# Optimization experiments

Measured on AMD Instinct MI355X. Metric: run time of the kernel, lower is better.

The kernel has to match this reference:

```python
import jax, jax.numpy as jnp
from jax import lax
import numpy as np

B, T, S, Q = 256, 128, 16, 16
E, K = 128, 20
VOCAB = 50000 + K  # vocab_size + num_blocks (key slots appended)


def prelu(x, a):
    return jnp.where(x > 0, x, a * x)


def setup_inputs() -> dict:
    key = jax.random.key(0)
    ks = jax.random.split(key, 12)
    story = jax.random.randint(ks[0], (B, T, S), 0, 50000, dtype=jnp.int64 if jax.config.jax_enable_x64 else jnp.int32)
    query = jax.random.randint(ks[1], (B, Q), 0, 50000, dtype=jnp.int64 if jax.config.jax_enable_x64 else jnp.int32)
    embed_table = jax.random.normal(ks[2], (VOCAB, E), jnp.float32) * 0.1
    embed_table = embed_table.at[0].set(0.0)  # padding_idx=0
    story_mask = jnp.ones((S, E), jnp.float32)
    query_mask = jnp.ones((Q, E), jnp.float32)
    prelu_a = jnp.ones((E,), jnp.float32)
    U = jax.random.normal(ks[3], (E, E), jnp.float32) * 0.1
    V = jax.random.normal(ks[4], (E, E), jnp.float32) * 0.1
    W = jax.random.normal(ks[5], (E, E), jnp.float32) * 0.1
    bias = jax.random.normal(ks[6], (E,), jnp.float32) * 0.1
    H = jax.random.normal(ks[7], (E, E), jnp.float32) * 0.1
    R = jax.random.normal(ks[8], (VOCAB, E), jnp.float32) * 0.1
    return {"story": story, "query": query, "embed_table": embed_table,
            "story_mask": story_mask, "query_mask": query_mask, "prelu_a": prelu_a,
            "U": U, "V": V, "W": W, "bias": bias, "H": H, "R": R}


def reference(story, query, embed_table, story_mask, query_mask, prelu_a, U, V, W, bias, H, R):
    # encode story: (B,T,S,E) * (S,E) summed over S -> (B,T,E)
    s_enc = jnp.sum(embed_table[story] * story_mask, axis=2)
    # encode query: (B,Q,E) * (Q,E) summed over Q -> (B,E)
    q_enc = jnp.sum(embed_table[query] * query_mask, axis=1)

    keys = embed_table[VOCAB - K:]              # (K,E) block keys
    state0 = jnp.broadcast_to(keys[None], (B, K, E))
    key_V = keys @ V.T                           # (K,E), loop-invariant

    def step(state, x):                          # state (B,K,E), x (B,E)
        gate = jax.nn.sigmoid(jnp.einsum('be,bke->bk', x, state) + x @ keys.T)  # (B,K)
        cand = prelu(jnp.einsum('bke,fe->bkf', state, U) + bias
                     + (x @ W.T)[:, None, :] + key_V[None], prelu_a)
        ns = state + gate[..., None] * cand
        norm = jnp.linalg.norm(ns, axis=-1, keepdims=True) + 1e-8
        ns = jnp.where(ns > 0, ns, 1.0) / norm   # Threshold(0,1) then L2-normalize
        return ns, None

    state, _ = lax.scan(step, state0, jnp.swapaxes(s_enc, 0, 1))  # scan over T

    # output module
    att = jax.nn.softmax(jnp.einsum('bke,be->bk', state, q_enc), axis=-1)
    u = jnp.einsum('bk,bke->be', att, state)
    y = prelu(q_enc + u @ H.T, prelu_a) @ R.T    # (B,VOCAB)
    return y
```

## Files before the change

kernel.cpp:

```cpp
#include <hip/hip_runtime.h>
#include <hip/hip_bf16.h>
#include <stdint.h>

#define BB 256
#define TT 128
#define SS 16
#define QQ 16
#define EE 128
#define KK 20
#define VOCAB 50020
#define KB_ROWS 10
#define XK_STR 24

#define NCVT  3127
#define NSTORY (BB*TT/8)
#define NQUERY (BB/8)

typedef __attribute__((ext_vector_type(8))) _Float16 h8v;
typedef __attribute__((ext_vector_type(2))) __fp16 fp2v;
typedef __attribute__((ext_vector_type(4))) unsigned short u4h;
typedef __attribute__((ext_vector_type(4))) float f4v;
#define MFMA16(a,b,c) __builtin_amdgcn_mfma_f32_16x16x32_f16(a,b,c,0,0,0)

static __device__ __forceinline__ unsigned pk2u(fp2v h){
  union { fp2v h; unsigned u; } c; c.h = h; return c.u;
}
static __device__ __forceinline__ float pk_lo(fp2v h){ return (float)h[0]; }
static __device__ __forceinline__ float pk_hi(fp2v h){ return (float)h[1]; }
static __device__ __forceinline__ unsigned short h1u(_Float16 h){
  union { _Float16 h; unsigned short u; } c; c.h = h; return c.u;
}
static __device__ __forceinline__ void split2_8(const float* v, h8v& h, h8v& l){
  #pragma unroll
  for (int j=0;j<8;++j){
    _Float16 hb = (_Float16)v[j];
    float hf = (float)hb;
    h[j] = hb;
    l[j] = (_Float16)(v[j]-hf);
  }
}
static __device__ __forceinline__ float dpp_add16(float x){
  int v;
  v = __builtin_amdgcn_update_dpp(0, __float_as_int(x), 0xB1, 0xF, 0xF, true);
  x += __int_as_float(v);
  v = __builtin_amdgcn_update_dpp(0, __float_as_int(x), 0x4E, 0xF, 0xF, true);
  x += __int_as_float(v);
  v = __builtin_amdgcn_update_dpp(0, __float_as_int(x), 0x124, 0xF, 0xF, true);
  x += __int_as_float(v);
  v = __builtin_amdgcn_update_dpp(0, __float_as_int(x), 0x128, 0xF, 0xF, true);
  x += __int_as_float(v);
  return x;
}
template<int IMM>
static __device__ __forceinline__ u4h tr_read(unsigned va){
  u4h d;
  asm volatile("ds_read_b64_tr_b16 %0, %1 offset:%c2" : "=v"(d) : "v"(va), "i"(IMM));
  return d;
}
static __device__ __forceinline__ h8v cat8h(u4h a, u4h b){
  union { u4h p[2]; h8v v; } u; u.p[0]=a; u.p[1]=b; return u.v;
}
#define LDA(P,K4) cat8h(tr_read<(P)*4096+(K4)*1024>(va), tr_read<(P)*4096+(K4)*1024+128>(va))

static const size_t OFF_SENC = 0;
static const size_t OFF_QENC = OFF_SENC + (size_t)BB*TT*EE;
static const size_t OFF_CKF  = OFF_QENC + (size_t)BB*EE;
static const size_t OFF_XW   = OFF_CKF  + (size_t)KK*EE;
static const size_t OFF_Z    = OFF_XW   + (size_t)BB*TT*EE;
static const size_t OFF_XK   = OFF_Z    + (size_t)BB*EE;
static const size_t OFF_ST   = OFF_XK   + (size_t)BB*TT*XK_STR;
static const size_t OFF_RH   = OFF_ST   + (size_t)BB*KK*EE;

__global__ __launch_bounds__(256) void k_pro(
    const int* __restrict__ story, const int* __restrict__ query,
    const float* __restrict__ emb, const float* __restrict__ smask,
    const float* __restrict__ qmask, const float* __restrict__ V,
    const float* __restrict__ bias, const float* __restrict__ R,
    float* __restrict__ senc, float* __restrict__ qenc,
    float* __restrict__ Ckf, unsigned short* __restrict__ Rh)
{
  int bid = blockIdx.x;
  int tid = threadIdx.x;
  if (bid < NCVT){
    size_t i = ((size_t)bid*256 + tid)*8;
    if (i >= (size_t)VOCAB*EE) return;
    float tmp[8];
    *(float4*)&tmp[0] = *(const float4*)(R+i);
    *(float4*)&tmp[4] = *(const float4*)(R+i+4);
    h8v h;
    #pragma unroll
    for (int j=0;j<8;++j) h[j] = (_Float16)tmp[j];
    *(h8v*)(Rh+i) = h;
  } else if (bid < NCVT + NSTORY){
    int row = (bid - NCVT)*8 + (tid>>5);
    int e4 = (tid&31)*4;
    float4 acc = make_float4(0.f,0.f,0.f,0.f);
    #pragma unroll
    for (int s=0; s<SS; ++s) {
      int id = story[(size_t)row*SS + s];
      float4 ev = *(const float4*)(emb + (size_t)id*EE + e4);
      float4 mv = *(const float4*)(smask + s*EE + e4);
      acc.x += ev.x*mv.x; acc.y += ev.y*mv.y; acc.z += ev.z*mv.z; acc.w += ev.w*mv.w;
    }
    *(float4*)(senc + (size_t)row*EE + e4) = acc;
  } else if (bid < NCVT + NSTORY + NQUERY){
    int row = (bid - NCVT - NSTORY)*8 + (tid>>5);
    int e4 = (tid&31)*4;
    float4 acc = make_float4(0.f,0.f,0.f,0.f);
    #pragma unroll
    for (int s=0; s<QQ; ++s) {
      int id = query[(size_t)row*QQ + s];
      float4 ev = *(const float4*)(emb + (size_t)id*EE + e4);
      float4 mv = *(const float4*)(qmask + s*EE + e4);
      acc.x += ev.x*mv.x; acc.y += ev.y*mv.y; acc.z += ev.z*mv.z; acc.w += ev.w*mv.w;
    }
    *(float4*)(qenc + (size_t)row*EE + e4) = acc;
  } else {
    int k = bid - NCVT - NSTORY - NQUERY;
    if (tid < 128){
      int f = tid;
      const float* key = emb + (size_t)(VOCAB-KK+k)*EE;
      const float* vr  = V + (size_t)f*EE;
      float acc = bias[f];
      for (int e=0; e<EE; e+=4) {
        float4 kv = *(const float4*)(key + e);
        float4 vv = *(const float4*)(vr + e);
        acc += kv.x*vv.x + kv.y*vv.y + kv.z*vv.z + kv.w*vv.w;
      }
      Ckf[k*EE + f] = acc;
    }
  }
}

__global__ __launch_bounds__(256) void k_xw(
    const float* __restrict__ senc, const float* __restrict__ W,
    const float* __restrict__ emb, float* __restrict__ xw,
    float* __restrict__ xk)
{
  __shared__ float xs[64*EE];
  __shared__ float keys_s[KK*EE];
  int tid = threadIdx.x;
  int r0 = blockIdx.x*64;
  for (int i=0;i<8;++i){
    int idx = tid + i*256; int r = idx>>5; int c4 = (idx&31)*4;
    *(float4*)(xs + r*EE + c4) = *(const float4*)(senc + (size_t)(r0+r)*EE + c4);
  }
  for (int idx=tid; idx<KK*EE; idx+=256)
    keys_s[idx] = emb[(size_t)(VOCAB-KK + (idx>>7))*EE + (idx&127)];
  __syncthreads();
  int f  = tid & 127;
  int rh = tid >> 7;
  float acc[32];
  #pragma unroll
  for (int i=0;i<32;++i) acc[i]=0.f;
  const float* wr = W + (size_t)f*EE;
  for (int e4=0; e4<EE; e4+=4) {
    float4 w4 = *(const float4*)(wr + e4);
    #pragma unroll
    for (int rr=0; rr<32; ++rr) {
      float4 x4 = *(const float4*)(xs + (rh*32+rr)*EE + e4);
      acc[rr] += w4.x*x4.x + w4.y*x4.y + w4.z*x4.z + w4.w*x4.w;
    }
  }
  #pragma unroll
  for (int rr=0; rr<32; ++rr)
    xw[(size_t)(r0 + rh*32 + rr)*EE + f] = acc[rr];
  for (int i=0;i<5;++i){
    int task = tid + i*256;
    int r = task/KK, k = task - r*KK;
    float a = 0.f;
    for (int e=0; e<EE; e+=4){
      float4 x4 = *(const float4*)(xs + r*EE + e);
      float4 k4 = *(const float4*)(keys_s + k*EE + e);
      a += x4.x*k4.x + x4.y*k4.y + x4.z*k4.z + x4.w*k4.w;
    }
    int ki = k < 10 ? k : k + 2;
    xk[(size_t)(r0+r)*XK_STR + ki] = a;
  }
}

struct ScanLds {
  unsigned short st[2][2][EE][16];
  unsigned short xp[2][2][EE];
  float npart[2][4][16];
};

__global__ __launch_bounds__(256) void k_scan(
    const float* __restrict__ emb, const float* __restrict__ U,
    const float* __restrict__ senc, const float* __restrict__ xw,
    const float* __restrict__ xk, const float* __restrict__ Ckf,
    const float* __restrict__ prelu_a, float* __restrict__ zst)
{
  __shared__ ScanLds L;
  int tid = threadIdx.x;
  int bid = blockIdx.x;
  int b   = bid >> 1, kb = bid & 1;
  int l   = tid & 63, cg = tid >> 6;
  int q   = l >> 4,  c  = l & 15;
  int col[2] = { cg*32 + c, cg*32 + 16 + c };

  for (int idx = tid; idx < 2*2*EE*16; idx += 256) ((unsigned short*)L.st)[idx] = 0;
  __syncthreads();
  for (int idx = tid; idx < KB_ROWS*EE; idx += 256){
    int row = idx >> 7, e = idx & 127;
    float v = emb[(size_t)(VOCAB - KK + kb*KB_ROWS + row)*EE + e];
    _Float16 hb = (_Float16)v;
    _Float16 lb = (_Float16)(v - (float)hb);
    L.st[0][0][e][row] = h1u(hb);
    L.st[0][1][e][row] = h1u(lb);
  }
  h8v bh[2][4], bl[2][4];
  #pragma unroll
  for (int nt=0;nt<2;++nt)
    #pragma unroll
    for (int kk=0;kk<4;++kk){
      float tmp[8];
      const float* up = U + (size_t)col[nt]*EE + kk*32 + q*8;
      *(float4*)&tmp[0] = *(const float4*)up;
      *(float4*)&tmp[4] = *(const float4*)(up+4);
      split2_8(tmp, bh[nt][kk], bl[nt][kk]);
    }
  float Creg[2][4], pa2[2], nsv[2][4];
  bool realr[4];
  #pragma unroll
  for (int r=0;r<4;++r) realr[r] = (4*q + r) < KB_ROWS;
  #pragma unroll
  for (int nt=0;nt<2;++nt){
    pa2[nt] = prelu_a[col[nt]];
    #pragma unroll
    for (int r=0;r<4;++r){
      int lr = 4*q + r;
      Creg[nt][r] = realr[r] ? Ckf[(kb*KB_ROWS+lr)*EE + col[nt]] : 0.f;
      nsv[nt][r]  = realr[r] ? emb[(size_t)(VOCAB-KK+kb*KB_ROWS+lr)*EE + col[nt]] : 0.f;
    }
  }

  const float* xrow  = senc + (size_t)b*TT*EE;
  const float* xwrow = xw   + (size_t)b*TT*EE;
  const float* xkrow = xk   + (size_t)b*TT*XK_STR + kb*12;

  if (tid < EE){
    float v = xrow[tid];
    _Float16 hb = (_Float16)v;
    _Float16 lb = (_Float16)(v - (float)hb);
    L.xp[0][0][tid] = h1u(hb); L.xp[0][1][tid] = h1u(lb);
  }
  float xwc[2] = { xwrow[col[0]], xwrow[col[1]] };
  float xkc[4];
  {
    f4v xk4 = {0.f,0.f,0.f,0.f};
    if (q < 3) xk4 = *(const f4v*)(xkrow + 4*q);
    #pragma unroll
    for (int r=0;r<4;++r) xkc[r] = realr[r] ? xk4[r] : 0.f;
  }

  unsigned va0 = (unsigned)(uintptr_t)&L.st[0][0][0][0] + q*256 + c*8;
  __syncthreads();

  for (int t=0; t<TT; ++t){
    int p = t & 1, pn = p ^ 1;
    unsigned va = va0 + p*8192;
    const unsigned short (*xpp)[EE] = L.xp[p];

    float invr[4];
    if (t > 0){
      f4v p0 = *(const f4v*)&L.npart[p][0][4*q];
      f4v p1 = *(const f4v*)&L.npart[p][1][4*q];
      f4v p2 = *(const f4v*)&L.npart[p][2][4*q];
      f4v p3 = *(const f4v*)&L.npart[p][3][4*q];
      f4v ss = p0 + p1 + p2 + p3;
      #pragma unroll
      for (int r=0;r<4;++r)
        invr[r] = __builtin_amdgcn_rcpf(__builtin_amdgcn_sqrtf(ss[r]) + 1e-8f);
    } else {
      #pragma unroll
      for (int r=0;r<4;++r) invr[r] = 1.0f;
    }

    float nxv = 0.f, xwn[2] = {0.f,0.f};
    f4v xk4n = {0.f,0.f,0.f,0.f};
    if (t+1 < TT){
      if (tid < EE) nxv = xrow[(size_t)(t+1)*EE + tid];
      xwn[0] = xwrow[(size_t)(t+1)*EE + col[0]];
      xwn[1] = xwrow[(size_t)(t+1)*EE + col[1]];
      if (q < 3) xk4n = *(const f4v*)(xkrow + (size_t)(t+1)*XK_STR + 4*q);
    }

    h8v Ah[4] = { LDA(0,0), LDA(0,1), LDA(0,2), LDA(0,3) };
    h8v Al[4] = { LDA(1,0), LDA(1,1), LDA(1,2), LDA(1,3) };
    asm volatile("s_waitcnt lgkmcnt(0)" ::: "memory");
    __builtin_amdgcn_sched_barrier(0);

    f4v z4 = {0.f,0.f,0.f,0.f};
    f4v acc[2][2] = {{z4,z4},{z4,z4}};
    f4v gac[2] = {z4,z4};
    #pragma unroll
    for (int kk=0; kk<4; ++kk){
      int h = kk>>1;
      h8v xh = *(const h8v*)&xpp[0][kk*32 + q*8];
      h8v xl = *(const h8v*)&xpp[1][kk*32 + q*8];
      #pragma unroll
      for (int nt=0;nt<2;++nt){
        acc[nt][h] = MFMA16(Al[kk], bh[nt][kk], acc[nt][h]);
        acc[nt][h] = MFMA16(Ah[kk], bl[nt][kk], acc[nt][h]);
        acc[nt][h] = MFMA16(Ah[kk], bh[nt][kk], acc[nt][h]);
      }
      gac[h] = MFMA16(Al[kk], xh, gac[h]);
      gac[h] = MFMA16(Ah[kk], xl, gac[h]);
      gac[h] = MFMA16(Ah[kk], xh, gac[h]);
    }
    f4v acc0 = acc[0][0] + acc[0][1];
    f4v acc1 = acc[1][0] + acc[1][1];
    f4v gacc = gac[0] + gac[1];

    float s2[4];
    #pragma unroll
    for (int r=0;r<4;++r){
      float graw = gacc[r]*invr[r] + xkc[r];
      float g = __builtin_amdgcn_rcpf(1.0f + __builtin_amdgcn_exp2f(-1.442695040889f * graw));
      float s2r = 0.f;
      #pragma unroll
      for (int nt=0;nt<2;++nt){
        float so = nsv[nt][r] * invr[r];
        float cv = (nt ? acc1[r] : acc0[r])*invr[r] + Creg[nt][r] + xwc[nt];
        cv = cv > 0.f ? cv : pa2[nt]*cv;
        float n = so + g*cv;
        nsv[nt][r] = realr[r] ? (n > 0.f ? n : 1.0f) : 0.f;
        s2r += n*n;
      }
      s2[r] = dpp_add16(s2r);
    }
    if (c == 0){
      f4v np; np[0]=s2[0]; np[1]=s2[1]; np[2]=s2[2]; np[3]=s2[3];
      *(f4v*)&L.npart[pn][cg][4*q] = np;
    }

    #pragma unroll
    for (int nt=0;nt<2;++nt){
      float v0=nsv[nt][0], v1=nsv[nt][1], v2=nsv[nt][2], v3=nsv[nt][3];
      fp2v pa = __builtin_amdgcn_cvt_pkrtz(v0, v1);
      fp2v pb = __builtin_amdgcn_cvt_pkrtz(v2, v3);
      float r0 = v0 - pk_lo(pa);
      float r1 = v1 - pk_hi(pa);
      float r2 = v2 - pk_lo(pb);
      float r3 = v3 - pk_hi(pb);
      fp2v pc = __builtin_amdgcn_cvt_pkrtz(r0, r1);
      fp2v pd = __builtin_amdgcn_cvt_pkrtz(r2, r3);
      *(uint2*)&L.st[pn][0][col[nt]][4*q] = make_uint2(pk2u(pa), pk2u(pb));
      *(uint2*)&L.st[pn][1][col[nt]][4*q] = make_uint2(pk2u(pc), pk2u(pd));
    }
    if (t+1 < TT && tid < EE){
      _Float16 hb = (_Float16)nxv;
      _Float16 lb = (_Float16)(nxv - (float)hb);
      L.xp[pn][0][tid] = h1u(hb); L.xp[pn][1][tid] = h1u(lb);
    }
    xwc[0]=xwn[0]; xwc[1]=xwn[1];
    #pragma unroll
    for (int r=0;r<4;++r) xkc[r] = realr[r] ? xk4n[r] : 0.f;
    __syncthreads();
  }

  {
    int pf = TT & 1;
    f4v p0 = *(const f4v*)&L.npart[pf][0][4*q];
    f4v p1 = *(const f4v*)&L.npart[pf][1][4*q];
    f4v p2 = *(const f4v*)&L.npart[pf][2][4*q];
    f4v p3 = *(const f4v*)&L.npart[pf][3][4*q];
    f4v ss = p0 + p1 + p2 + p3;
    #pragma unroll
    for (int r=0;r<4;++r){
      if (realr[r]){
        float inv = __builtin_amdgcn_rcpf(__builtin_amdgcn_sqrtf(ss[r]) + 1e-8f);
        #pragma unroll
        for (int nt=0;nt<2;++nt)
          zst[((size_t)b*KK + kb*KB_ROWS + 4*q + r)*EE + col[nt]] = nsv[nt][r]*inv;
      }
    }
  }
}

__global__ __launch_bounds__(128) void k_tail(
    const float* __restrict__ zst, const float* __restrict__ qenc,
    const float* __restrict__ prelu_a, const float* __restrict__ H,
    float* __restrict__ zout)
{
  __shared__ float st[KK*EE];
  __shared__ float us[EE];
  __shared__ float red[2][KK];
  __shared__ float gs[KK];
  int b = blockIdx.x, tid = threadIdx.x;
  for (int i = tid; i < KK*EE; i += 128) st[i] = zst[(size_t)b*KK*EE + i];
  float qv = qenc[(size_t)b*EE + tid];
  __syncthreads();
  int wv = tid >> 6, ln = tid & 63;
  for (int k=0;k<KK;++k){
    float p = qv * st[k*EE + tid];
    #pragma unroll
    for (int off=32; off; off>>=1) p += __shfl_xor(p, off);
    if (ln == 0) red[wv][k] = p;
  }
  __syncthreads();
  if (tid == 0){
    float mx = -1e30f, gg[KK];
    for (int k=0;k<KK;++k){ float v = red[0][k]+red[1][k]; gg[k]=v; mx = fmaxf(mx, v); }
    float s = 0.f;
    for (int k=0;k<KK;++k){ float e_ = expf(gg[k]-mx); gg[k]=e_; s += e_; }
    for (int k=0;k<KK;++k) gs[k] = gg[k]/s;
  }
  __syncthreads();
  float u_ = 0.f;
  #pragma unroll
  for (int k=0;k<KK;++k) u_ += gs[k]*st[k*EE + tid];
  us[tid] = u_;
  __syncthreads();
  float hp = 0.f;
  const float* hr = H + (size_t)tid*EE;
  for (int e=0; e<EE; e+=4){
    float4 h4 = *(const float4*)(hr + e);
    float4 u4 = *(const float4*)(us + e);
    hp += h4.x*u4.x + h4.y*u4.y + h4.z*u4.z + h4.w*u4.w;
  }
  float zv = qv + hp;
  float pat = prelu_a[tid];
  zv = zv > 0.f ? zv : pat*zv;
  zout[(size_t)b*EE + tid] = zv;
}

__global__ __launch_bounds__(256) void k_out(
    const float* __restrict__ z, const unsigned short* __restrict__ Rh,
    float* __restrict__ y)
{
  int tid = threadIdx.x;
  int w = tid >> 6, l = tid & 63;
  int q = l >> 4, cc = l & 15;
  int b0 = blockIdx.y * 64;
  int vbase = blockIdx.x * 256 + w * 64;

  h8v ah[4][4], al[4][4];
  #pragma unroll
  for (int mt=0;mt<4;++mt){
    const float* zr = z + (size_t)(b0 + mt*16 + cc)*EE;
    #pragma unroll
    for (int kk=0;kk<4;++kk){
      float tmp[8];
      *(float4*)&tmp[0] = *(const float4*)(zr + kk*32 + q*8);
      *(float4*)&tmp[4] = *(const float4*)(zr + kk*32 + q*8 + 4);
      split2_8(tmp, ah[mt][kk], al[mt][kk]);
    }
  }
  #pragma unroll
  for (int vt=0; vt<4; ++vt){
    int v = vbase + vt*16 + cc;
    int vc = v < VOCAB ? v : VOCAB-1;
    const unsigned short* rr = Rh + (size_t)vc*EE;
    h8v bh[4];
    #pragma unroll
    for (int kk=0;kk<4;++kk)
      bh[kk] = *(const h8v*)(rr + kk*32 + q*8);
    f4v acc0 = {0.f,0.f,0.f,0.f};
    f4v acc1 = {0.f,0.f,0.f,0.f};
    f4v acc2 = {0.f,0.f,0.f,0.f};
    f4v acc3 = {0.f,0.f,0.f,0.f};
    #pragma unroll
    for (int kk=0;kk<4;++kk){
      acc0 = MFMA16(al[0][kk], bh[kk], acc0);
      acc0 = MFMA16(ah[0][kk], bh[kk], acc0);
      acc1 = MFMA16(al[1][kk], bh[kk], acc1);
      acc1 = MFMA16(ah[1][kk], bh[kk], acc1);
      acc2 = MFMA16(al[2][kk], bh[kk], acc2);
      acc2 = MFMA16(ah[2][kk], bh[kk], acc2);
      acc3 = MFMA16(al[3][kk], bh[kk], acc3);
      acc3 = MFMA16(ah[3][kk], bh[kk], acc3);
    }
    if (v < VOCAB){
      #pragma unroll
      for (int r=0;r<4;++r){
        y[(size_t)(b0 +      q*4 + r)*VOCAB + v] = acc0[r];
        y[(size_t)(b0 + 16 + q*4 + r)*VOCAB + v] = acc1[r];
        y[(size_t)(b0 + 32 + q*4 + r)*VOCAB + v] = acc2[r];
        y[(size_t)(b0 + 48 + q*4 + r)*VOCAB + v] = acc3[r];
      }
    }
  }
}

extern "C" void kernel_launch(void* const* d_in, const int* in_sizes, int n_in,
                              void* d_out, int out_size, void* d_ws, size_t ws_size,
                              hipStream_t stream)
{
  const int*   story = (const int*)d_in[0];
  const int*   query = (const int*)d_in[1];
  const float* emb   = (const float*)d_in[2];
  const float* smask = (const float*)d_in[3];
  const float* qmask = (const float*)d_in[4];
  const float* pa    = (const float*)d_in[5];
  const float* U     = (const float*)d_in[6];
  const float* V     = (const float*)d_in[7];
  const float* W     = (const float*)d_in[8];
  const float* bias  = (const float*)d_in[9];
  const float* H     = (const float*)d_in[10];
  const float* R     = (const float*)d_in[11];
  float* y  = (float*)d_out;
  float* ws = (float*)d_ws;

  float* s_enc = ws + OFF_SENC;
  float* q_enc = ws + OFF_QENC;
  float* Ckf   = ws + OFF_CKF;
  float* xw    = ws + OFF_XW;
  float* z     = ws + OFF_Z;
  float* xk    = ws + OFF_XK;
  float* zst   = ws + OFF_ST;
  unsigned short* Rh = (unsigned short*)(ws + OFF_RH);

  k_pro<<<dim3(NCVT + NSTORY + NQUERY + KK), 256, 0, stream>>>(
      story, query, emb, smask, qmask, V, bias, R, s_enc, q_enc, Ckf, Rh);
  k_xw<<<dim3(BB*TT/64), 256, 0, stream>>>(s_enc, W, emb, xw, xk);

  k_scan<<<dim3(BB*2), 256, 0, stream>>>(emb, U, s_enc, xw, xk, Ckf, pa, zst);
  k_tail<<<dim3(BB), 128, 0, stream>>>(zst, q_enc, pa, H, z);

  k_out<<<dim3((VOCAB+255)/256, BB/64), 256, 0, stream>>>(z, Rh, y);
}
```

Measured before the change: 363.5 us.

## Spread scan columns over eight waves with one N-tile per wave

The recurrent scan kernel moves from 4 waves that each handle two 16-column N-tiles to 8 waves that each handle one, so the block grows to 512 threads. This halves the serial MFMA chain and elementwise work per wave on every time step, aiming to shorten the latency-bound loop. In exchange, the gate MFMAs are now computed redundantly in 8 waves instead of 4, the norm reduction reads 8 partials, and the per-step block barrier must synchronise twice as many waves.

```diff
diff --git a/kernel.cpp b/kernel.cpp
--- a/kernel.cpp
+++ b/kernel.cpp
@@ -182,10 +182,10 @@
 struct ScanLds {
   unsigned short st[2][2][EE][16];
   unsigned short xp[2][2][EE];
-  float npart[2][4][16];
+  float npart[2][8][16];
 };
 
-__global__ __launch_bounds__(256) void k_scan(
+__global__ __launch_bounds__(512) void k_scan(
     const float* __restrict__ emb, const float* __restrict__ U,
     const float* __restrict__ senc, const float* __restrict__ xw,
     const float* __restrict__ xk, const float* __restrict__ Ckf,
@@ -195,13 +195,13 @@
   int tid = threadIdx.x;
   int bid = blockIdx.x;
   int b   = bid >> 1, kb = bid & 1;
-  int l   = tid & 63, cg = tid >> 6;
+  int l   = tid & 63, w = tid >> 6;
   int q   = l >> 4,  c  = l & 15;
-  int col[2] = { cg*32 + c, cg*32 + 16 + c };
-
-  for (int idx = tid; idx < 2*2*EE*16; idx += 256) ((unsigned short*)L.st)[idx] = 0;
-  __syncthreads();
-  for (int idx = tid; idx < KB_ROWS*EE; idx += 256){
+  int col = w*16 + c;
+
+  for (int idx = tid; idx < 2*2*EE*16; idx += 512) ((unsigned short*)L.st)[idx] = 0;
+  __syncthreads();
+  for (int idx = tid; idx < KB_ROWS*EE; idx += 512){
     int row = idx >> 7, e = idx & 127;
     float v = emb[(size_t)(VOCAB - KK + kb*KB_ROWS + row)*EE + e];
     _Float16 hb = (_Float16)v;
@@ -209,30 +209,25 @@
     L.st[0][0][e][row] = h1u(hb);
     L.st[0][1][e][row] = h1u(lb);
   }
-  h8v bh[2][4], bl[2][4];
-  #pragma unroll
-  for (int nt=0;nt<2;++nt)
-    #pragma unroll
-    for (int kk=0;kk<4;++kk){
-      float tmp[8];
-      const float* up = U + (size_t)col[nt]*EE + kk*32 + q*8;
-      *(float4*)&tmp[0] = *(const float4*)up;
-      *(float4*)&tmp[4] = *(const float4*)(up+4);
-      split2_8(tmp, bh[nt][kk], bl[nt][kk]);
-    }
-  float Creg[2][4], pa2[2], nsv[2][4];
+  h8v bh[4], bl[4];
+  #pragma unroll
+  for (int kk=0;kk<4;++kk){
+    float tmp[8];
+    const float* up = U + (size_t)col*EE + kk*32 + q*8;
+    *(float4*)&tmp[0] = *(const float4*)up;
+    *(float4*)&tmp[4] = *(const float4*)(up+4);
+    split2_8(tmp, bh[kk], bl[kk]);
+  }
+  float Creg[4], nsv[4];
   bool realr[4];
   #pragma unroll
   for (int r=0;r<4;++r) realr[r] = (4*q + r) < KB_ROWS;
-  #pragma unroll
-  for (int nt=0;nt<2;++nt){
-    pa2[nt] = prelu_a[col[nt]];
-    #pragma unroll
-    for (int r=0;r<4;++r){
-      int lr = 4*q + r;
-      Creg[nt][r] = realr[r] ? Ckf[(kb*KB_ROWS+lr)*EE + col[nt]] : 0.f;
-      nsv[nt][r]  = realr[r] ? emb[(size_t)(VOCAB-KK+kb*KB_ROWS+lr)*EE + col[nt]] : 0.f;
-    }
+  float pa2 = prelu_a[col];
+  #pragma unroll
+  for (int r=0;r<4;++r){
+    int lr = 4*q + r;
+    Creg[r] = realr[r] ? Ckf[(kb*KB_ROWS+lr)*EE + col] : 0.f;
+    nsv[r]  = realr[r] ? emb[(size_t)(VOCAB-KK+kb*KB_ROWS+lr)*EE + col] : 0.f;
   }
 
   const float* xrow  = senc + (size_t)b*TT*EE;
@@ -245,7 +240,7 @@
     _Float16 lb = (_Float16)(v - (float)hb);
     L.xp[0][0][tid] = h1u(hb); L.xp[0][1][tid] = h1u(lb);
   }
-  float xwc[2] = { xwrow[col[0]], xwrow[col[1]] };
+  float xwc = xwrow[col];
   float xkc[4];
   {
     f4v xk4 = {0.f,0.f,0.f,0.f};
@@ -264,11 +259,9 @@
 
     float invr[4];
     if (t > 0){
-      f4v p0 = *(const f4v*)&L.npart[p][0][4*q];
-      f4v p1 = *(const f4v*)&L.npart[p][1][4*q];
-      f4v p2 = *(const f4v*)&L.npart[p][2][4*q];
-      f4v p3 = *(const f4v*)&L.npart[p][3][4*q];
-      f4v ss = p0 + p1 + p2 + p3;
+      f4v ss = *(const f4v*)&L.npart[p][0][4*q];
+      #pragma unroll
+      for (int g=1; g<8; ++g) ss += *(const f4v*)&L.npart[p][g][4*q];
       #pragma unroll
       for (int r=0;r<4;++r)
         invr[r] = __builtin_amdgcn_rcpf(__builtin_amdgcn_sqrtf(ss[r]) + 1e-8f);
@@ -277,12 +270,11 @@
       for (int r=0;r<4;++r) invr[r] = 1.0f;
     }
 
-    float nxv = 0.f, xwn[2] = {0.f,0.f};
+    float nxv = 0.f, xwn = 0.f;
     f4v xk4n = {0.f,0.f,0.f,0.f};
     if (t+1 < TT){
       if (tid < EE) nxv = xrow[(size_t)(t+1)*EE + tid];
-      xwn[0] = xwrow[(size_t)(t+1)*EE + col[0]];
-      xwn[1] = xwrow[(size_t)(t+1)*EE + col[1]];
+      xwn = xwrow[(size_t)(t+1)*EE + col];
       if (q < 3) xk4n = *(const f4v*)(xkrow + (size_t)(t+1)*XK_STR + 4*q);
     }
 
@@ -292,25 +284,21 @@
     __builtin_amdgcn_sched_barrier(0);
 
     f4v z4 = {0.f,0.f,0.f,0.f};
-    f4v acc[2][2] = {{z4,z4},{z4,z4}};
+    f4v acch[2] = {z4,z4};
     f4v gac[2] = {z4,z4};
     #pragma unroll
     for (int kk=0; kk<4; ++kk){
       int h = kk>>1;
       h8v xh = *(const h8v*)&xpp[0][kk*32 + q*8];
       h8v xl = *(const h8v*)&xpp[1][kk*32 + q*8];
-      #pragma unroll
-      for (int nt=0;nt<2;++nt){
-        acc[nt][h] = MFMA16(Al[kk], bh[nt][kk], acc[nt][h]);
-        acc[nt][h] = MFMA16(Ah[kk], bl[nt][kk], acc[nt][h]);
-        acc[nt][h] = MFMA16(Ah[kk], bh[nt][kk], acc[nt][h]);
-      }
+      acch[h] = MFMA16(Al[kk], bh[kk], acch[h]);
+      acch[h] = MFMA16(Ah[kk], bl[kk], acch[h]);
+      acch[h] = MFMA16(Ah[kk], bh[kk], acch[h]);
       gac[h] = MFMA16(Al[kk], xh, gac[h]);
       gac[h] = MFMA16(Ah[kk], xl, gac[h]);
       gac[h] = MFMA16(Ah[kk], xh, gac[h]);
     }
-    f4v acc0 = acc[0][0] + acc[0][1];
-    f4v acc1 = acc[1][0] + acc[1][1];
+    f4v accs = acch[0] + acch[1];
     f4v gacc = gac[0] + gac[1];
 
     float s2[4];
@@ -318,26 +306,20 @@
     for (int r=0;r<4;++r){
       float graw = gacc[r]*invr[r] + xkc[r];
       float g = __builtin_amdgcn_rcpf(1.0f + __builtin_amdgcn_exp2f(-1.442695040889f * graw));
-      float s2r = 0.f;
-      #pragma unroll
-      for (int nt=0;nt<2;++nt){
-        float so = nsv[nt][r] * invr[r];
-        float cv = (nt ? acc1[r] : acc0[r])*invr[r] + Creg[nt][r] + xwc[nt];
-        cv = cv > 0.f ? cv : pa2[nt]*cv;
-        float n = so + g*cv;
-        nsv[nt][r] = realr[r] ? (n > 0.f ? n : 1.0f) : 0.f;
-        s2r += n*n;
-      }
-      s2[r] = dpp_add16(s2r);
+      float so = nsv[r] * invr[r];
+      float cv = accs[r]*invr[r] + Creg[r] + xwc;
+      cv = cv > 0.f ? cv : pa2*cv;
+      float n = so + g*cv;
+      nsv[r] = realr[r] ? (n > 0.f ? n : 1.0f) : 0.f;
+      s2[r] = dpp_add16(n*n);
     }
     if (c == 0){
       f4v np; np[0]=s2[0]; np[1]=s2[1]; np[2]=s2[2]; np[3]=s2[3];
-      *(f4v*)&L.npart[pn][cg][4*q] = np;
-    }
-
-    #pragma unroll
-    for (int nt=0;nt<2;++nt){
-      float v0=nsv[nt][0], v1=nsv[nt][1], v2=nsv[nt][2], v3=nsv[nt][3];
+      *(f4v*)&L.npart[pn][w][4*q] = np;
+    }
+
+    {
+      float v0=nsv[0], v1=nsv[1], v2=nsv[2], v3=nsv[3];
       fp2v pa = __builtin_amdgcn_cvt_pkrtz(v0, v1);
       fp2v pb = __builtin_amdgcn_cvt_pkrtz(v2, v3);
       float r0 = v0 - pk_lo(pa);
@@ -346,15 +328,15 @@
       float r3 = v3 - pk_hi(pb);
       fp2v pc = __builtin_amdgcn_cvt_pkrtz(r0, r1);
       fp2v pd = __builtin_amdgcn_cvt_pkrtz(r2, r3);
-      *(uint2*)&L.st[pn][0][col[nt]][4*q] = make_uint2(pk2u(pa), pk2u(pb));
-      *(uint2*)&L.st[pn][1][col[nt]][4*q] = make_uint2(pk2u(pc), pk2u(pd));
+      *(uint2*)&L.st[pn][0][col][4*q] = make_uint2(pk2u(pa), pk2u(pb));
+      *(uint2*)&L.st[pn][1][col][4*q] = make_uint2(pk2u(pc), pk2u(pd));
     }
     if (t+1 < TT && tid < EE){
       _Float16 hb = (_Float16)nxv;
       _Float16 lb = (_Float16)(nxv - (float)hb);
       L.xp[pn][0][tid] = h1u(hb); L.xp[pn][1][tid] = h1u(lb);
     }
-    xwc[0]=xwn[0]; xwc[1]=xwn[1];
+    xwc = xwn;
     #pragma unroll
     for (int r=0;r<4;++r) xkc[r] = realr[r] ? xk4n[r] : 0.f;
     __syncthreads();
@@ -362,18 +344,14 @@
 
   {
     int pf = TT & 1;
-    f4v p0 = *(const f4v*)&L.npart[pf][0][4*q];
-    f4v p1 = *(const f4v*)&L.npart[pf][1][4*q];
-    f4v p2 = *(const f4v*)&L.npart[pf][2][4*q];
-    f4v p3 = *(const f4v*)&L.npart[pf][3][4*q];
-    f4v ss = p0 + p1 + p2 + p3;
+    f4v ss = *(const f4v*)&L.npart[pf][0][4*q];
+    #pragma unroll
+    for (int g=1; g<8; ++g) ss += *(const f4v*)&L.npart[pf][g][4*q];
     #pragma unroll
     for (int r=0;r<4;++r){
       if (realr[r]){
         float inv = __builtin_amdgcn_rcpf(__builtin_amdgcn_sqrtf(ss[r]) + 1e-8f);
-        #pragma unroll
-        for (int nt=0;nt<2;++nt)
-          zst[((size_t)b*KK + kb*KB_ROWS + 4*q + r)*EE + col[nt]] = nsv[nt][r]*inv;
+        zst[((size_t)b*KK + kb*KB_ROWS + 4*q + r)*EE + col] = nsv[r]*inv;
       }
     }
   }
@@ -516,7 +494,7 @@
       story, query, emb, smask, qmask, V, bias, R, s_enc, q_enc, Ckf, Rh);
   k_xw<<<dim3(BB*TT/64), 256, 0, stream>>>(s_enc, W, emb, xw, xk);
 
-  k_scan<<<dim3(BB*2), 256, 0, stream>>>(emb, U, s_enc, xw, xk, Ckf, pa, zst);
+  k_scan<<<dim3(BB*2), 512, 0, stream>>>(emb, U, s_enc, xw, xk, Ckf, pa, zst);
   k_tail<<<dim3(BB), 128, 0, stream>>>(zst, q_enc, pa, H, z);
 
   k_out<<<dim3((VOCAB+255)/256, BB/64), 256, 0, stream>>>(z, Rh, y);
```

New measurement: 492.2 us. +35.4%, slower.
